# Performance work log

Measured on AMD Instinct MI355X. Metric: run time of the kernel, lower is better.

The kernel has to match this reference:

```python
import jax, jax.numpy as jnp
import numpy as np

B, S, D, H, DFF = 4, 2048, 512, 8, 2048
DK = D // H
EPS = 1e-6
NEG = -1.0e9


def _linear(x, w, b):
    return x @ w.T + b


def _layernorm(x, gamma, bias):
    # torch.var default is unbiased (ddof=1); gamma/bias are scalars
    mean = jnp.mean(x, axis=-1, keepdims=True)
    var = jnp.var(x, axis=-1, keepdims=True, ddof=1)
    return gamma * (x - mean) / jnp.sqrt(var + EPS) + bias


def setup_inputs() -> dict:
    key = jax.random.key(0)
    ks = jax.random.split(key, 16)
    sc = 0.02
    inp = {
        "x": jax.random.normal(ks[0], (B, S, D), jnp.float32),
        "mask": jax.random.randint(ks[1], (B, 1, 1, S), 0, 2).astype(jnp.bool_),
        "wq": jax.random.normal(ks[2], (D, D), jnp.float32) * sc,
        "bq": jnp.zeros((D,), jnp.float32),
        "wk": jax.random.normal(ks[3], (D, D), jnp.float32) * sc,
        "bk": jnp.zeros((D,), jnp.float32),
        "wv": jax.random.normal(ks[4], (D, D), jnp.float32) * sc,
        "bv": jnp.zeros((D,), jnp.float32),
        "wo": jax.random.normal(ks[5], (D, D), jnp.float32) * sc,
        "bo": jnp.zeros((D,), jnp.float32),
        "w1": jax.random.normal(ks[6], (DFF, D), jnp.float32) * sc,
        "b1": jnp.zeros((DFF,), jnp.float32),
        "w2": jax.random.normal(ks[7], (D, DFF), jnp.float32) * sc,
        "b2": jnp.zeros((D,), jnp.float32),
        "g1": jnp.ones((), jnp.float32),
        "beta1": jnp.zeros((), jnp.float32),
        "g2": jnp.ones((), jnp.float32),
        "beta2": jnp.zeros((), jnp.float32),
    }
    return inp


def reference(x, mask, wq, bq, wk, bk, wv, bv, wo, bo, w1, b1, w2, b2, g1, beta1, g2, beta2):
    # --- multi-head self-attention ---
    q = _linear(x, wq, bq).reshape(B, S, H, DK)
    k = _linear(x, wk, bk).reshape(B, S, H, DK)
    v = _linear(x, wv, bv).reshape(B, S, H, DK)
    scores = jnp.einsum("bqhd,bkhd->bhqk", q, k) / jnp.sqrt(jnp.float32(DK))
    scores = jnp.where(mask, NEG, scores)  # masked_fill_ where mask is True
    attn = jax.nn.softmax(scores, axis=-1)
    o = jnp.einsum("bhqk,bkhd->bqhd", attn, v).reshape(B, S, D)
    attn_out = _linear(o, wo, bo)
    # skip connection 1: x + norm(sublayer_out)  (dropout = identity at inference)
    y = x + _layernorm(attn_out, g1, beta1)
    # --- feed-forward ---
    ff = _linear(jax.nn.relu(_linear(y, w1, b1)), w2, b2)
    # skip connection 2
    return y + _layernorm(ff, g2, beta2)
```

## Files before the change

### kernel.cpp

```cpp
#include <hip/hip_runtime.h>
#include <hip/hip_bf16.h>
#include <math.h>

#define B_ 4
#define S_ 2048
#define D_ 512
#define H_ 8
#define DK_ 64
#define DFF_ 2048
#define NEG_ (-1.0e9f)
#define EPS_ 1e-6f

typedef __attribute__((ext_vector_type(8))) short bf16x8;
typedef __attribute__((ext_vector_type(4))) float f32x4;

__device__ inline unsigned short f2bf(float f) {
    unsigned u = __float_as_uint(f);
    unsigned r = u + 0x7FFFu + ((u >> 16) & 1u);
    return (unsigned short)(r >> 16);
}

__device__ inline f32x4 mfma16(bf16x8 a, bf16x8 b, f32x4 c) {
    return __builtin_amdgcn_mfma_f32_16x16x32_bf16(a, b, c, 0, 0, 0);
}

__device__ inline void gload16(const void* g, void* l) {
    __builtin_amdgcn_global_load_lds(
        (const __attribute__((address_space(1))) unsigned int*)g,
        (__attribute__((address_space(3))) unsigned int*)l, 16, 0, 0);
}
__device__ inline void gload4(const void* g, void* l) {
    __builtin_amdgcn_global_load_lds(
        (const __attribute__((address_space(1))) unsigned int*)g,
        (__attribute__((address_space(3))) unsigned int*)l, 4, 0, 0);
}

__global__ void mask_canon_kernel(const unsigned char* __restrict__ mraw,
                                  float* __restrict__ mb) {
    __shared__ int s_bad;
    int tid = threadIdx.x;
    if (tid == 0) s_bad = 0;
    __syncthreads();
    const unsigned int* w = (const unsigned int*)mraw;
    int bad = 0;
    for (int i = tid; i < (B_ * S_) / 4; i += 256) {
        unsigned int v = w[i];
        if (!(v == 0u || v == 1u || v == 0x3F800000u)) bad = 1;
    }
    if (bad) atomicOr(&s_bad, 1);
    __syncthreads();
    if (s_bad) {
        for (int i = tid; i < B_ * S_; i += 256) mb[i] = mraw[i] ? NEG_ : 0.f;
    } else {
        for (int i = tid; i < B_ * S_; i += 256) mb[i] = w[i] ? NEG_ : 0.f;
    }
}

__global__ __launch_bounds__(256) void f32_to_bf16_kernel(
    const float* __restrict__ src, unsigned short* __restrict__ dst, int n4) {
    int i = blockIdx.x * 256 + threadIdx.x;
    if (i < n4) {
        float4 v = reinterpret_cast<const float4*>(src)[i];
        ushort4 o;
        o.x = f2bf(v.x); o.y = f2bf(v.y); o.z = f2bf(v.z); o.w = f2bf(v.w);
        reinterpret_cast<ushort4*>(dst)[i] = o;
    }
}

template<int BM, int BN, bool RELU, bool OUT_BF16>
__global__ __launch_bounds__(256) void gemm_mfma(
    const unsigned short* __restrict__ A, const unsigned short* __restrict__ W,
    const float* __restrict__ bias, void* __restrict__ Cout,
    int M, int N, int K)
{
    constexpr int FM = BM / 32;
    constexpr int FN = BN / 32;
    __shared__ unsigned short Asl[BM * 64];
    __shared__ unsigned short Bsl[BN * 64];

    const int tid = threadIdx.x;
    const int w = tid >> 6, lane = tid & 63;
    const int lr = lane & 15, lg = lane >> 4;
    const int wm = w >> 1, wn = w & 1;
    const int m0 = blockIdx.y * BM, n0 = blockIdx.x * BN;
    const int srow = lane >> 3;
    const int schunk = lane & 7;

    f32x4 acc[FM][FN] = {};

    for (int k0 = 0; k0 < K; k0 += 64) {
        __syncthreads();
        #pragma unroll
        for (int j = 0; j < BM / 32; ++j) {
            int instr = w * (BM / 32) + j;
            int row = instr * 8 + srow;
            const unsigned short* src =
                A + (size_t)(m0 + row) * K + k0 + ((schunk ^ (row & 7)) * 8);
            gload16(src, &Asl[instr * 512]);
        }
        #pragma unroll
        for (int j = 0; j < BN / 32; ++j) {
            int instr = w * (BN / 32) + j;
            int row = instr * 8 + srow;
            const unsigned short* src =
                W + (size_t)(n0 + row) * K + k0 + ((schunk ^ (row & 7)) * 8);
            gload16(src, &Bsl[instr * 512]);
        }
        __syncthreads();

        bf16x8 af[FM][2], bfr[FN][2];
        #pragma unroll
        for (int m = 0; m < FM; ++m)
            #pragma unroll
            for (int ko = 0; ko < 2; ++ko) {
                int row = wm * (FM * 16) + m * 16 + lr;
                int slot = (lg + 4 * ko) ^ (row & 7);
                af[m][ko] = *(const bf16x8*)&Asl[row * 64 + slot * 8];
            }
        #pragma unroll
        for (int n = 0; n < FN; ++n)
            #pragma unroll
            for (int ko = 0; ko < 2; ++ko) {
                int row = wn * (FN * 16) + n * 16 + lr;
                int slot = (lg + 4 * ko) ^ (row & 7);
                bfr[n][ko] = *(const bf16x8*)&Bsl[row * 64 + slot * 8];
            }
        #pragma unroll
        for (int m = 0; m < FM; ++m)
            #pragma unroll
            for (int n = 0; n < FN; ++n)
                #pragma unroll
                for (int ko = 0; ko < 2; ++ko)
                    acc[m][n] = mfma16(af[m][ko], bfr[n][ko], acc[m][n]);
    }

    #pragma unroll
    for (int n = 0; n < FN; ++n) {
        int col = n0 + wn * (FN * 16) + n * 16 + lr;
        float bv = bias[col];
        #pragma unroll
        for (int m = 0; m < FM; ++m) {
            int rowb = m0 + wm * (FM * 16) + m * 16 + lg * 4;
            #pragma unroll
            for (int r = 0; r < 4; ++r) {
                float v = acc[m][n][r] + bv;
                if (RELU) v = fmaxf(v, 0.f);
                if (OUT_BF16)
                    ((unsigned short*)Cout)[(size_t)(rowb + r) * N + col] = f2bf(v);
                else
                    ((float*)Cout)[(size_t)(rowb + r) * N + col] = v;
            }
        }
    }
}

__global__ __launch_bounds__(256) void gemm_qkv(
    const unsigned short* __restrict__ A, const unsigned short* __restrict__ W,
    const float* __restrict__ bias, unsigned short* __restrict__ QKb,
    unsigned short* __restrict__ VTg)
{
    constexpr int K = 512;
    __shared__ unsigned short Asl[128 * 64];
    __shared__ unsigned short Bsl[128 * 64];

    const int tid = threadIdx.x;
    const int w = tid >> 6, lane = tid & 63;
    const int lr = lane & 15, lg = lane >> 4;
    const int wm = w >> 1, wn = w & 1;
    const int m0 = blockIdx.y * 128, n0 = blockIdx.x * 128;
    const int srow = lane >> 3;
    const int schunk = lane & 7;

    f32x4 acc[4][4] = {};

    for (int k0 = 0; k0 < K; k0 += 64) {
        __syncthreads();
        #pragma unroll
        for (int j = 0; j < 4; ++j) {
            int instr = w * 4 + j;
            int row = instr * 8 + srow;
            gload16(A + (size_t)(m0 + row) * K + k0 + ((schunk ^ (row & 7)) * 8),
                    &Asl[instr * 512]);
            gload16(W + (size_t)(n0 + row) * K + k0 + ((schunk ^ (row & 7)) * 8),
                    &Bsl[instr * 512]);
        }
        __syncthreads();

        bf16x8 af[4][2], bfr[4][2];
        #pragma unroll
        for (int m = 0; m < 4; ++m)
            #pragma unroll
            for (int ko = 0; ko < 2; ++ko) {
                int row = wm * 64 + m * 16 + lr;
                int slot = (lg + 4 * ko) ^ (row & 7);
                af[m][ko] = *(const bf16x8*)&Asl[row * 64 + slot * 8];
            }
        #pragma unroll
        for (int n = 0; n < 4; ++n)
            #pragma unroll
            for (int ko = 0; ko < 2; ++ko) {
                int row = wn * 64 + n * 16 + lr;
                int slot = (lg + 4 * ko) ^ (row & 7);
                bfr[n][ko] = *(const bf16x8*)&Bsl[row * 64 + slot * 8];
            }
        #pragma unroll
        for (int m = 0; m < 4; ++m)
            #pragma unroll
            for (int n = 0; n < 4; ++n)
                #pragma unroll
                for (int ko = 0; ko < 2; ++ko)
                    acc[m][n] = mfma16(af[m][ko], bfr[n][ko], acc[m][n]);
    }

    if (n0 < 1024) {
        #pragma unroll
        for (int n = 0; n < 4; ++n) {
            int col = n0 + wn * 64 + n * 16 + lr;
            float bv = bias[col];
            #pragma unroll
            for (int m = 0; m < 4; ++m) {
                int rowb = m0 + wm * 64 + m * 16 + lg * 4;
                #pragma unroll
                for (int r = 0; r < 4; ++r)
                    QKb[(size_t)(rowb + r) * 1024 + col] = f2bf(acc[m][n][r] + bv);
            }
        }
    } else {
        #pragma unroll
        for (int n = 0; n < 4; ++n) {
            int col = n0 + wn * 64 + n * 16 + lr;
            int dfull = col - 1024;
            int hh = dfull >> 6, dd = dfull & 63;
            float bv = bias[col];
            #pragma unroll
            for (int m = 0; m < 4; ++m) {
                int rowb = m0 + wm * 64 + m * 16 + lg * 4;
                int bb = rowb >> 11;
                int s = rowb & 2047;
                ushort4 pk;
                pk.x = f2bf(acc[m][n][0] + bv);
                pk.y = f2bf(acc[m][n][1] + bv);
                pk.z = f2bf(acc[m][n][2] + bv);
                pk.w = f2bf(acc[m][n][3] + bv);
                *(ushort4*)&VTg[(((size_t)bb * 8 + hh) * 64 + dd) * 2048 + s] = pk;
            }
        }
    }
}

__global__ __launch_bounds__(256, 2) void attn_mfma2(
    const unsigned short* __restrict__ QKb, const unsigned short* __restrict__ VTg,
    const float* __restrict__ mb, unsigned short* __restrict__ Ob)
{
    __shared__ unsigned short Ks[64 * 64];
    __shared__ unsigned short VTs[64 * 64];
    __shared__ unsigned short Ps[4 * 32 * 64];
    __shared__ float Ms[64];

    const int tid = threadIdx.x;
    const int w = tid >> 6, lane = tid & 63;
    const int lr = lane & 15, lg = lane >> 4;
    const int q0 = blockIdx.x * 128;
    const int h = blockIdx.y, b = blockIdx.z;
    const int srow = lane >> 3;
    const int sc_x = (lane & 7) ^ srow;
    const int bh = b * H_ + h;
    unsigned short* PsW = &Ps[w * 2048];

    bf16x8 qf[2][2];
    #pragma unroll
    for (int qb = 0; qb < 2; ++qb)
        #pragma unroll
        for (int ko = 0; ko < 2; ++ko)
            qf[qb][ko] = *(const bf16x8*)(QKb +
                (size_t)(b * S_ + q0 + w * 32 + qb * 16 + lr) * 1024 +
                h * 64 + ko * 32 + lg * 8);

    f32x4 od[2][4] = {};
    float m_run[2] = {-INFINITY, -INFINITY};
    float l_run[2] = {0.f, 0.f};

    for (int kv0 = 0; kv0 < S_; kv0 += 64) {
        __syncthreads();
        #pragma unroll
        for (int j = 0; j < 2; ++j) {
            int rl = w * 16 + j * 8 + srow;
            gload16(QKb + (size_t)(b * S_ + kv0 + rl) * 1024 + 512 + h * 64 + sc_x * 8,
                    &Ks[(w * 2 + j) * 512]);
            gload16(VTg + ((size_t)bh * 64 + rl) * 2048 + kv0 + sc_x * 8,
                    &VTs[(w * 2 + j) * 512]);
        }
        if (w == 0) gload4(mb + (size_t)b * S_ + kv0 + lane, Ms);
        __syncthreads();

        f32x4 st[4][2] = {};
        #pragma unroll
        for (int ko = 0; ko < 2; ++ko)
            #pragma unroll
            for (int n = 0; n < 4; ++n) {
                bf16x8 kf = *(const bf16x8*)
                    &Ks[(n * 16 + lr) * 64 + (((lg + 4 * ko) ^ (lr & 7)) * 8)];
                st[n][0] = mfma16(kf, qf[0][ko], st[n][0]);
                st[n][1] = mfma16(kf, qf[1][ko], st[n][1]);
            }

        f32x4 mbr[4];
        #pragma unroll
        for (int n = 0; n < 4; ++n)
            mbr[n] = *(const f32x4*)&Ms[n * 16 + lg * 4];

        #pragma unroll
        for (int qb = 0; qb < 2; ++qb) {
            float mt = -INFINITY;
            #pragma unroll
            for (int n = 0; n < 4; ++n)
                #pragma unroll
                for (int r = 0; r < 4; ++r) {
                    float v = st[n][qb][r] * 0.125f + mbr[n][r];
                    st[n][qb][r] = v;
                    mt = fmaxf(mt, v);
                }
            mt = fmaxf(mt, __shfl_xor(mt, 16));
            mt = fmaxf(mt, __shfl_xor(mt, 32));
            float mnew = fmaxf(m_run[qb], mt);
            float scl = __expf(m_run[qb] - mnew);
            m_run[qb] = mnew;
            float psum = 0.f;
            #pragma unroll
            for (int n = 0; n < 4; ++n) {
                float p0 = __expf(st[n][qb][0] - mnew);
                float p1 = __expf(st[n][qb][1] - mnew);
                float p2 = __expf(st[n][qb][2] - mnew);
                float p3 = __expf(st[n][qb][3] - mnew);
                psum += (p0 + p1) + (p2 + p3);
                ushort4 pk;
                pk.x = f2bf(p0); pk.y = f2bf(p1); pk.z = f2bf(p2); pk.w = f2bf(p3);
                int chunk = (2 * n + (lg >> 1)) ^ (lr & 7);
                *(ushort4*)&PsW[(qb * 16 + lr) * 64 + chunk * 8 + (lg & 1) * 4] = pk;
            }
            psum += __shfl_xor(psum, 16);
            psum += __shfl_xor(psum, 32);
            l_run[qb] = l_run[qb] * scl + psum;
            #pragma unroll
            for (int r = 0; r < 4; ++r) {
                float sr = __shfl(scl, lg * 4 + r);
                #pragma unroll
                for (int nd = 0; nd < 4; ++nd) od[qb][nd][r] *= sr;
            }
        }

        #pragma unroll
        for (int ko = 0; ko < 2; ++ko) {
            int slotx = ((lg + 4 * ko) ^ (lr & 7)) * 8;
            bf16x8 pa0 = *(const bf16x8*)&PsW[(0  + lr) * 64 + slotx];
            bf16x8 pa1 = *(const bf16x8*)&PsW[(16 + lr) * 64 + slotx];
            #pragma unroll
            for (int nd = 0; nd < 4; ++nd) {
                bf16x8 vf = *(const bf16x8*)&VTs[(nd * 16 + lr) * 64 + slotx];
                od[0][nd] = mfma16(pa0, vf, od[0][nd]);
                od[1][nd] = mfma16(pa1, vf, od[1][nd]);
            }
        }
    }

    #pragma unroll
    for (int qb = 0; qb < 2; ++qb) {
        float linv = 1.f / l_run[qb];
        #pragma unroll
        for (int r = 0; r < 4; ++r) {
            float iv = __shfl(linv, lg * 4 + r);
            size_t row = (size_t)(b * S_ + q0 + w * 32 + qb * 16 + lg * 4 + r);
            #pragma unroll
            for (int nd = 0; nd < 4; ++nd)
                Ob[row * 512 + h * 64 + nd * 16 + lr] = f2bf(od[qb][nd][r] * iv);
        }
    }
}

__global__ __launch_bounds__(256) void add_ln_kernel(
    const float* __restrict__ x, const float* __restrict__ a,
    const float* __restrict__ g, const float* __restrict__ beta,
    float* __restrict__ y, unsigned short* __restrict__ ybf)
{
    int rowid = blockIdx.x;
    int tid = threadIdx.x;
    const float2 a2 = reinterpret_cast<const float2*>(a + (size_t)rowid * D_)[tid];
    float s = a2.x + a2.y;
    float ss = a2.x * a2.x + a2.y * a2.y;
    #pragma unroll
    for (int off = 32; off > 0; off >>= 1) {
        s += __shfl_down(s, off);
        ss += __shfl_down(ss, off);
    }
    __shared__ float ws_s[4], ws_ss[4];
    __shared__ float s_mean, s_rstd;
    int wave = tid >> 6, lane = tid & 63;
    if (lane == 0) { ws_s[wave] = s; ws_ss[wave] = ss; }
    __syncthreads();
    if (tid == 0) {
        float st = ws_s[0] + ws_s[1] + ws_s[2] + ws_s[3];
        float sst = ws_ss[0] + ws_ss[1] + ws_ss[2] + ws_ss[3];
        float mean = st / (float)D_;
        float var = (sst - (float)D_ * mean * mean) / (float)(D_ - 1);
        s_mean = mean;
        s_rstd = rsqrtf(var + EPS_);
    }
    __syncthreads();
    float mean = s_mean, rstd = s_rstd, gg = g[0], bb = beta[0];
    const float2 x2 = reinterpret_cast<const float2*>(x + (size_t)rowid * D_)[tid];
    float2 o;
    o.x = x2.x + gg * (a2.x - mean) * rstd + bb;
    o.y = x2.y + gg * (a2.y - mean) * rstd + bb;
    reinterpret_cast<float2*>(y + (size_t)rowid * D_)[tid] = o;
    if (ybf) {
        ushort2 ob; ob.x = f2bf(o.x); ob.y = f2bf(o.y);
        reinterpret_cast<ushort2*>(ybf + (size_t)rowid * D_)[tid] = ob;
    }
}

extern "C" void kernel_launch(void* const* d_in, const int* in_sizes, int n_in,
                              void* d_out, int out_size, void* d_ws, size_t ws_size,
                              hipStream_t stream) {
    const float* x  = (const float*)d_in[0];
    const unsigned char* mask = (const unsigned char*)d_in[1];
    const float* wq = (const float*)d_in[2];
    const float* bq = (const float*)d_in[3];
    const float* wk = (const float*)d_in[4];
    const float* bk = (const float*)d_in[5];
    const float* wv = (const float*)d_in[6];
    const float* bv = (const float*)d_in[7];
    const float* wo = (const float*)d_in[8];
    const float* bo = (const float*)d_in[9];
    const float* w1 = (const float*)d_in[10];
    const float* b1 = (const float*)d_in[11];
    const float* w2 = (const float*)d_in[12];
    const float* b2 = (const float*)d_in[13];
    const float* g1 = (const float*)d_in[14];
    const float* be1 = (const float*)d_in[15];
    const float* g2 = (const float*)d_in[16];
    const float* be2 = (const float*)d_in[17];
    float* out = (float*)d_out;
    char* base = (char*)d_ws;

    const size_t MS = (size_t)B_ * S_;
    unsigned short* QKb  = (unsigned short*)(base);
    unsigned short* VTg  = (unsigned short*)(base + 16777216);
    unsigned short* Ob   = (unsigned short*)(base + 25165824);
    unsigned short* ff1  = (unsigned short*)(base);
    float*          att  = (float*)(base + 33554432);
    float*          ff2  = att;
    float*          y    = (float*)(base + 50331648);
    unsigned short* ybf  = (unsigned short*)(base + 67108864);
    unsigned short* xb   = (unsigned short*)(base + 75497472);
    unsigned short* wqkvb= (unsigned short*)(base + 83886080);
    unsigned short* wob  = (unsigned short*)(base + 85458944);
    unsigned short* w1b  = (unsigned short*)(base + 85983232);
    unsigned short* w2b  = (unsigned short*)(base + 88080384);
    float*          bqkv = (float*)(base + 90177536);
    float*          mb   = (float*)(base + 90183680);

    dim3 blk(256);
    mask_canon_kernel<<<1, blk, 0, stream>>>(mask, mb);

    f32_to_bf16_kernel<<<(B_*S_*D_/4 + 255)/256, blk, 0, stream>>>(x, xb, B_*S_*D_/4);
    f32_to_bf16_kernel<<<(D_*D_/4 + 255)/256, blk, 0, stream>>>(wq, wqkvb,           D_*D_/4);
    f32_to_bf16_kernel<<<(D_*D_/4 + 255)/256, blk, 0, stream>>>(wk, wqkvb + D_*D_,   D_*D_/4);
    f32_to_bf16_kernel<<<(D_*D_/4 + 255)/256, blk, 0, stream>>>(wv, wqkvb + 2*D_*D_, D_*D_/4);
    f32_to_bf16_kernel<<<(D_*D_/4 + 255)/256, blk, 0, stream>>>(wo, wob, D_*D_/4);
    f32_to_bf16_kernel<<<(DFF_*D_/4 + 255)/256, blk, 0, stream>>>(w1, w1b, DFF_*D_/4);
    f32_to_bf16_kernel<<<(DFF_*D_/4 + 255)/256, blk, 0, stream>>>(w2, w2b, DFF_*D_/4);

    hipMemcpyAsync(bqkv,        bq, D_ * sizeof(float), hipMemcpyDeviceToDevice, stream);
    hipMemcpyAsync(bqkv + D_,   bk, D_ * sizeof(float), hipMemcpyDeviceToDevice, stream);
    hipMemcpyAsync(bqkv + 2*D_, bv, D_ * sizeof(float), hipMemcpyDeviceToDevice, stream);

    gemm_qkv<<<dim3(12, MS / 128), blk, 0, stream>>>(xb, wqkvb, bqkv, QKb, VTg);

    attn_mfma2<<<dim3(S_ / 128, H_, B_), blk, 0, stream>>>(QKb, VTg, mb, Ob);

    gemm_mfma<128,64,false,false><<<dim3(D_/64, MS/128), blk, 0, stream>>>(
        Ob, wob, bo, att, MS, D_, D_);

    add_ln_kernel<<<dim3((unsigned)MS), blk, 0, stream>>>(x, att, g1, be1, y, ybf);

    gemm_mfma<128,128,true,true><<<dim3(DFF_/128, MS/128), blk, 0, stream>>>(
        ybf, w1b, b1, ff1, MS, DFF_, D_);
    gemm_mfma<128,64,false,false><<<dim3(D_/64, MS/128), blk, 0, stream>>>(
        ff1, w2b, b2, ff2, MS, D_, DFF_);

    add_ln_kernel<<<dim3((unsigned)MS), blk, 0, stream>>>(y, ff2, g2, be2, out, nullptr);
}
```

Measured before the change: 333.1 us.

## Fuse conversions, fold softmax scale into Wq, and shrink attention tiles

```diff
diff --git a/kernel.cpp b/kernel.cpp
--- a/kernel.cpp
+++ b/kernel.cpp
@@ -49,22 +49,36 @@
     }
     if (bad) atomicOr(&s_bad, 1);
     __syncthreads();
+    int i = blockIdx.x * 256 + tid;
     if (s_bad) {
-        for (int i = tid; i < B_ * S_; i += 256) mb[i] = mraw[i] ? NEG_ : 0.f;
+        for (; i < B_ * S_; i += 2048) mb[i] = mraw[i] ? NEG_ : 0.f;
     } else {
-        for (int i = tid; i < B_ * S_; i += 256) mb[i] = w[i] ? NEG_ : 0.f;
-    }
-}
-
-__global__ __launch_bounds__(256) void f32_to_bf16_kernel(
-    const float* __restrict__ src, unsigned short* __restrict__ dst, int n4) {
+        for (; i < B_ * S_; i += 2048) mb[i] = w[i] ? NEG_ : 0.f;
+    }
+}
+
+__global__ __launch_bounds__(256) void convert_all_kernel(
+    const float* __restrict__ x,  const float* __restrict__ wq,
+    const float* __restrict__ wk, const float* __restrict__ wv,
+    const float* __restrict__ wo, const float* __restrict__ w1,
+    const float* __restrict__ w2,
+    unsigned short* __restrict__ xb, unsigned short* __restrict__ wqkvb,
+    unsigned short* __restrict__ wob, unsigned short* __restrict__ w1b,
+    unsigned short* __restrict__ w2b)
+{
     int i = blockIdx.x * 256 + threadIdx.x;
-    if (i < n4) {
-        float4 v = reinterpret_cast<const float4*>(src)[i];
-        ushort4 o;
-        o.x = f2bf(v.x); o.y = f2bf(v.y); o.z = f2bf(v.z); o.w = f2bf(v.w);
-        reinterpret_cast<ushort4*>(dst)[i] = o;
-    }
+    const float* src; unsigned short* dst; int off; float s = 1.f;
+    if (i < 1048576)      { src = x;  dst = xb;             off = i;           }
+    else if (i < 1114112) { src = wq; dst = wqkvb;          off = i - 1048576; s = 0.125f; }
+    else if (i < 1179648) { src = wk; dst = wqkvb + 262144; off = i - 1114112; }
+    else if (i < 1245184) { src = wv; dst = wqkvb + 524288; off = i - 1179648; }
+    else if (i < 1310720) { src = wo; dst = wob;            off = i - 1245184; }
+    else if (i < 1572864) { src = w1; dst = w1b;            off = i - 1310720; }
+    else                  { src = w2; dst = w2b;            off = i - 1572864; }
+    float4 v = reinterpret_cast<const float4*>(src)[off];
+    ushort4 o;
+    o.x = f2bf(v.x * s); o.y = f2bf(v.y * s); o.z = f2bf(v.z * s); o.w = f2bf(v.w * s);
+    reinterpret_cast<ushort4*>(dst)[off] = o;
 }
 
 template<int BM, int BN, bool RELU, bool OUT_BF16>
@@ -156,7 +170,8 @@
 
 __global__ __launch_bounds__(256) void gemm_qkv(
     const unsigned short* __restrict__ A, const unsigned short* __restrict__ W,
-    const float* __restrict__ bias, unsigned short* __restrict__ QKb,
+    const float* __restrict__ bqp, const float* __restrict__ bkp,
+    const float* __restrict__ bvp, unsigned short* __restrict__ QKb,
     unsigned short* __restrict__ VTg)
 {
     constexpr int K = 512;
@@ -216,7 +231,7 @@
         #pragma unroll
         for (int n = 0; n < 4; ++n) {
             int col = n0 + wn * 64 + n * 16 + lr;
-            float bv = bias[col];
+            float bv = (col < 512) ? bqp[col] * 0.125f : bkp[col - 512];
             #pragma unroll
             for (int m = 0; m < 4; ++m) {
                 int rowb = m0 + wm * 64 + m * 16 + lg * 4;
@@ -231,7 +246,7 @@
             int col = n0 + wn * 64 + n * 16 + lr;
             int dfull = col - 1024;
             int hh = dfull >> 6, dd = dfull & 63;
-            float bv = bias[col];
+            float bv = bvp[dfull];
             #pragma unroll
             for (int m = 0; m < 4; ++m) {
                 int rowb = m0 + wm * 64 + m * 16 + lg * 4;
@@ -248,37 +263,36 @@
     }
 }
 
-__global__ __launch_bounds__(256, 2) void attn_mfma2(
+__global__ __launch_bounds__(256, 4) void attn_mfma3(
     const unsigned short* __restrict__ QKb, const unsigned short* __restrict__ VTg,
     const float* __restrict__ mb, unsigned short* __restrict__ Ob)
 {
     __shared__ unsigned short Ks[64 * 64];
     __shared__ unsigned short VTs[64 * 64];
-    __shared__ unsigned short Ps[4 * 32 * 64];
+    __shared__ unsigned short Ps[4 * 16 * 64];
     __shared__ float Ms[64];
 
     const int tid = threadIdx.x;
     const int w = tid >> 6, lane = tid & 63;
     const int lr = lane & 15, lg = lane >> 4;
-    const int q0 = blockIdx.x * 128;
-    const int h = blockIdx.y, b = blockIdx.z;
+    const int flat = blockIdx.x + 32 * (blockIdx.y + 8 * blockIdx.z);
+    const int nf = (flat & 7) * 128 + (flat >> 3);
+    const int q0 = (nf & 31) * 64;
+    const int bh = nf >> 5;
+    const int h = bh & 7, b = bh >> 3;
     const int srow = lane >> 3;
     const int sc_x = (lane & 7) ^ srow;
-    const int bh = b * H_ + h;
-    unsigned short* PsW = &Ps[w * 2048];
-
-    bf16x8 qf[2][2];
+    unsigned short* PsW = &Ps[w * 1024];
+
+    bf16x8 qf[2];
     #pragma unroll
-    for (int qb = 0; qb < 2; ++qb)
-        #pragma unroll
-        for (int ko = 0; ko < 2; ++ko)
-            qf[qb][ko] = *(const bf16x8*)(QKb +
-                (size_t)(b * S_ + q0 + w * 32 + qb * 16 + lr) * 1024 +
-                h * 64 + ko * 32 + lg * 8);
-
-    f32x4 od[2][4] = {};
-    float m_run[2] = {-INFINITY, -INFINITY};
-    float l_run[2] = {0.f, 0.f};
+    for (int ko = 0; ko < 2; ++ko)
+        qf[ko] = *(const bf16x8*)(QKb +
+            (size_t)(b * S_ + q0 + w * 16 + lr) * 1024 + h * 64 + ko * 32 + lg * 8);
+
+    f32x4 od[4] = {};
+    float m_run = -INFINITY;
+    float l_run = 0.f;
 
     for (int kv0 = 0; kv0 < S_; kv0 += 64) {
         __syncthreads();
@@ -293,87 +307,81 @@
         if (w == 0) gload4(mb + (size_t)b * S_ + kv0 + lane, Ms);
         __syncthreads();
 
-        f32x4 st[4][2] = {};
+        f32x4 st[4] = {};
         #pragma unroll
         for (int ko = 0; ko < 2; ++ko)
             #pragma unroll
             for (int n = 0; n < 4; ++n) {
                 bf16x8 kf = *(const bf16x8*)
                     &Ks[(n * 16 + lr) * 64 + (((lg + 4 * ko) ^ (lr & 7)) * 8)];
-                st[n][0] = mfma16(kf, qf[0][ko], st[n][0]);
-                st[n][1] = mfma16(kf, qf[1][ko], st[n][1]);
-            }
-
-        f32x4 mbr[4];
-        #pragma unroll
-        for (int n = 0; n < 4; ++n)
-            mbr[n] = *(const f32x4*)&Ms[n * 16 + lg * 4];
-
-        #pragma unroll
-        for (int qb = 0; qb < 2; ++qb) {
-            float mt = -INFINITY;
-            #pragma unroll
-            for (int n = 0; n < 4; ++n)
-                #pragma unroll
-                for (int r = 0; r < 4; ++r) {
-                    float v = st[n][qb][r] * 0.125f + mbr[n][r];
-                    st[n][qb][r] = v;
-                    mt = fmaxf(mt, v);
-                }
+                st[n] = mfma16(kf, qf[ko], st[n]);
+            }
+
+        float mtp = -INFINITY;
+        #pragma unroll
+        for (int n = 0; n < 4; ++n) {
+            f32x4 mbr = *(const f32x4*)&Ms[n * 16 + lg * 4];
+            #pragma unroll
+            for (int r = 0; r < 4; ++r) {
+                float v = st[n][r] + mbr[r];
+                st[n][r] = v;
+                mtp = fmaxf(mtp, v);
+            }
+        }
+
+        if (__any(mtp > m_run + 4.f)) {
+            float mt = mtp;
             mt = fmaxf(mt, __shfl_xor(mt, 16));
             mt = fmaxf(mt, __shfl_xor(mt, 32));
-            float mnew = fmaxf(m_run[qb], mt);
-            float scl = __expf(m_run[qb] - mnew);
-            m_run[qb] = mnew;
-            float psum = 0.f;
-            #pragma unroll
-            for (int n = 0; n < 4; ++n) {
-                float p0 = __expf(st[n][qb][0] - mnew);
-                float p1 = __expf(st[n][qb][1] - mnew);
-                float p2 = __expf(st[n][qb][2] - mnew);
-                float p3 = __expf(st[n][qb][3] - mnew);
-                psum += (p0 + p1) + (p2 + p3);
-                ushort4 pk;
-                pk.x = f2bf(p0); pk.y = f2bf(p1); pk.z = f2bf(p2); pk.w = f2bf(p3);
-                int chunk = (2 * n + (lg >> 1)) ^ (lr & 7);
-                *(ushort4*)&PsW[(qb * 16 + lr) * 64 + chunk * 8 + (lg & 1) * 4] = pk;
-            }
-            psum += __shfl_xor(psum, 16);
-            psum += __shfl_xor(psum, 32);
-            l_run[qb] = l_run[qb] * scl + psum;
+            float mnew = fmaxf(m_run, mt);
+            float scl = __expf(m_run - mnew);
+            m_run = mnew;
+            l_run *= scl;
             #pragma unroll
             for (int r = 0; r < 4; ++r) {
                 float sr = __shfl(scl, lg * 4 + r);
                 #pragma unroll
-                for (int nd = 0; nd < 4; ++nd) od[qb][nd][r] *= sr;
-            }
-        }
+                for (int nd = 0; nd < 4; ++nd) od[nd][r] *= sr;
+            }
+        }
+
+        float psum = 0.f;
+        #pragma unroll
+        for (int n = 0; n < 4; ++n) {
+            float p0 = __expf(st[n][0] - m_run);
+            float p1 = __expf(st[n][1] - m_run);
+            float p2 = __expf(st[n][2] - m_run);
+            float p3 = __expf(st[n][3] - m_run);
+            psum += (p0 + p1) + (p2 + p3);
+            ushort4 pk;
+            pk.x = f2bf(p0); pk.y = f2bf(p1); pk.z = f2bf(p2); pk.w = f2bf(p3);
+            int chunk = (2 * n + (lg >> 1)) ^ (lr & 7);
+            *(ushort4*)&PsW[lr * 64 + chunk * 8 + (lg & 1) * 4] = pk;
+        }
+        psum += __shfl_xor(psum, 16);
+        psum += __shfl_xor(psum, 32);
+        l_run += psum;
 
         #pragma unroll
         for (int ko = 0; ko < 2; ++ko) {
             int slotx = ((lg + 4 * ko) ^ (lr & 7)) * 8;
-            bf16x8 pa0 = *(const bf16x8*)&PsW[(0  + lr) * 64 + slotx];
-            bf16x8 pa1 = *(const bf16x8*)&PsW[(16 + lr) * 64 + slotx];
+            bf16x8 pa = *(const bf16x8*)&PsW[lr * 64 + slotx];
             #pragma unroll
             for (int nd = 0; nd < 4; ++nd) {
                 bf16x8 vf = *(const bf16x8*)&VTs[(nd * 16 + lr) * 64 + slotx];
-                od[0][nd] = mfma16(pa0, vf, od[0][nd]);
-                od[1][nd] = mfma16(pa1, vf, od[1][nd]);
-            }
-        }
-    }
-
+                od[nd] = mfma16(pa, vf, od[nd]);
+            }
+        }
+    }
+
+    float linv = 1.f / l_run;
     #pragma unroll
-    for (int qb = 0; qb < 2; ++qb) {
-        float linv = 1.f / l_run[qb];
-        #pragma unroll
-        for (int r = 0; r < 4; ++r) {
-            float iv = __shfl(linv, lg * 4 + r);
-            size_t row = (size_t)(b * S_ + q0 + w * 32 + qb * 16 + lg * 4 + r);
-            #pragma unroll
-            for (int nd = 0; nd < 4; ++nd)
-                Ob[row * 512 + h * 64 + nd * 16 + lr] = f2bf(od[qb][nd][r] * iv);
-        }
+    for (int r = 0; r < 4; ++r) {
+        float iv = __shfl(linv, lg * 4 + r);
+        size_t row = (size_t)(b * S_ + q0 + w * 16 + lg * 4 + r);
+        #pragma unroll
+        for (int nd = 0; nd < 4; ++nd)
+            Ob[row * 512 + h * 64 + nd * 16 + lr] = f2bf(od[nd][r] * iv);
     }
 }
 
@@ -456,27 +464,18 @@
     unsigned short* wob  = (unsigned short*)(base + 85458944);
     unsigned short* w1b  = (unsigned short*)(base + 85983232);
     unsigned short* w2b  = (unsigned short*)(base + 88080384);
-    float*          bqkv = (float*)(base + 90177536);
-    float*          mb   = (float*)(base + 90183680);
+    float*          mbv  = (float*)(base + 90183680);
 
     dim3 blk(256);
-    mask_canon_kernel<<<1, blk, 0, stream>>>(mask, mb);
-
-    f32_to_bf16_kernel<<<(B_*S_*D_/4 + 255)/256, blk, 0, stream>>>(x, xb, B_*S_*D_/4);
-    f32_to_bf16_kernel<<<(D_*D_/4 + 255)/256, blk, 0, stream>>>(wq, wqkvb,           D_*D_/4);
-    f32_to_bf16_kernel<<<(D_*D_/4 + 255)/256, blk, 0, stream>>>(wk, wqkvb + D_*D_,   D_*D_/4);
-    f32_to_bf16_kernel<<<(D_*D_/4 + 255)/256, blk, 0, stream>>>(wv, wqkvb + 2*D_*D_, D_*D_/4);
-    f32_to_bf16_kernel<<<(D_*D_/4 + 255)/256, blk, 0, stream>>>(wo, wob, D_*D_/4);
-    f32_to_bf16_kernel<<<(DFF_*D_/4 + 255)/256, blk, 0, stream>>>(w1, w1b, DFF_*D_/4);
-    f32_to_bf16_kernel<<<(DFF_*D_/4 + 255)/256, blk, 0, stream>>>(w2, w2b, DFF_*D_/4);
-
-    hipMemcpyAsync(bqkv,        bq, D_ * sizeof(float), hipMemcpyDeviceToDevice, stream);
-    hipMemcpyAsync(bqkv + D_,   bk, D_ * sizeof(float), hipMemcpyDeviceToDevice, stream);
-    hipMemcpyAsync(bqkv + 2*D_, bv, D_ * sizeof(float), hipMemcpyDeviceToDevice, stream);
-
-    gemm_qkv<<<dim3(12, MS / 128), blk, 0, stream>>>(xb, wqkvb, bqkv, QKb, VTg);
-
-    attn_mfma2<<<dim3(S_ / 128, H_, B_), blk, 0, stream>>>(QKb, VTg, mb, Ob);
+    mask_canon_kernel<<<8, blk, 0, stream>>>(mask, mbv);
+
+    convert_all_kernel<<<7168, blk, 0, stream>>>(
+        x, wq, wk, wv, wo, w1, w2, xb, wqkvb, wob, w1b, w2b);
+
+    gemm_qkv<<<dim3(12, MS / 128), blk, 0, stream>>>(
+        xb, wqkvb, bq, bk, bv, QKb, VTg);
+
+    attn_mfma3<<<dim3(S_ / 64, H_, B_), blk, 0, stream>>>(QKb, VTg, mbv, Ob);
 
     gemm_mfma<128,64,false,false><<<dim3(D_/64, MS/128), blk, 0, stream>>>(
         Ob, wob, bo, att, MS, D_, D_);
```

Measured after the change: 296.8 us. 10.9% less time.
